# Performance work log

Measured on AMD Instinct MI355X. Metric: run time of the kernel, lower is better.

## Reference

```python
import jax, jax.numpy as jnp
from jax import lax
import numpy as np

H = 256  # hidden_size


def gru_last(x, Wih, Whh, bih, bhh):
    """Single-layer torch-convention GRU; returns last hidden state.
    x: [B, T, C] -> [B, H]"""
    B, T, _ = x.shape
    h_dim = Whh.shape[1]
    xW = x @ Wih.T + bih  # [B, T, 3H], precompute input gates
    def step(h, xw):
        gi_r, gi_z, gi_n = jnp.split(xw, 3, axis=-1)
        gh = h @ Whh.T + bhh
        gh_r, gh_z, gh_n = jnp.split(gh, 3, axis=-1)
        r = jax.nn.sigmoid(gi_r + gh_r)
        z = jax.nn.sigmoid(gi_z + gh_z)
        n = jnp.tanh(gi_n + r * gh_n)
        return (1.0 - z) * n + z * h, None
    h0 = jnp.zeros((B, h_dim), x.dtype)
    hT, _ = lax.scan(step, h0, jnp.swapaxes(xW, 0, 1))
    return hT


def setup_inputs() -> dict:
    key = jax.random.key(0)
    ks = jax.random.split(key, 16)
    B, N, M, C, C1 = 32, 64, 64, 64, 16
    inter = 2 * H + 6 * C + C1  # 912
    s = 0.05
    x1 = jax.random.normal(ks[0], (B, N, C1), jnp.float32)
    states = jax.random.normal(ks[1], (B, N, M, C), jnp.float32)
    perm1 = jax.vmap(lambda k: jax.random.permutation(k, M))(jax.random.split(ks[2], N)).astype(jnp.int64)
    perm2 = jax.vmap(lambda k: jax.random.permutation(k, N))(jax.random.split(ks[3], N)).astype(jnp.int64)
    return {
        "x1": x1, "states": states, "perm1": perm1, "perm2": perm2,
        # shared 2D->1D GRU (ModuleList([gru]*2) shares parameters)
        "gru2d_Wih": jax.random.normal(ks[4], (3 * H, C), jnp.float32) * s,
        "gru2d_Whh": jax.random.normal(ks[5], (3 * H, H), jnp.float32) * s,
        "gru2d_bih": jax.random.normal(ks[6], (3 * H,), jnp.float32) * s,
        "gru2d_bhh": jax.random.normal(ks[7], (3 * H,), jnp.float32) * s,
        "gru1d_Wih": jax.random.normal(ks[8], (3 * H, inter), jnp.float32) * s,
        "gru1d_Whh": jax.random.normal(ks[9], (3 * H, H), jnp.float32) * s,
        "gru1d_bih": jax.random.normal(ks[10], (3 * H,), jnp.float32) * s,
        "gru1d_bhh": jax.random.normal(ks[11], (3 * H,), jnp.float32) * s,
        "fc1_W": jax.random.normal(ks[12], (H, 3 * inter + H), jnp.float32) * s,
        "fc1_b": jax.random.normal(ks[13], (H,), jnp.float32) * s,
        "fc2_W": jax.random.normal(ks[14], (1, H), jnp.float32) * s,
        "fc2_b": jax.random.normal(ks[15], (1,), jnp.float32) * s,
    }


def reference(x1, states, perm1, perm2,
              gru2d_Wih, gru2d_Whh, gru2d_bih, gru2d_bhh,
              gru1d_Wih, gru1d_Whh, gru1d_bih, gru1d_bhh,
              fc1_W, fc1_b, fc2_W, fc2_b):
    B, N, M, C = states.shape
    d = [states.max(1), states.mean(1), states.min(1),   # [B, M, C] each (N==M)
         states.max(2), states.mean(2), states.min(2)]   # [B, N, C] each
    idx = jnp.arange(N)[:, None]
    # g1[b,i,t,c] = states[b, i, perm1[i,t], c]
    g1 = states[:, idx, perm1, :]                         # [B, N, M, C]
    # g2[b,i,t,c] = states[b, perm2[i,t], i, c]
    g2 = states[:, perm2, idx, :]                         # [B, N, N, C]
    sd1 = gru_last(g1.reshape(B * N, M, C), gru2d_Wih, gru2d_Whh, gru2d_bih, gru2d_bhh).reshape(B, N, H)
    sd2 = gru_last(g2.reshape(B * N, N, C), gru2d_Wih, gru2d_Whh, gru2d_bih, gru2d_bhh).reshape(B, N, H)
    f = jnp.concatenate(d + [sd1, sd2], axis=2)           # [B, N, 6C + 2H]
    f = jnp.concatenate([x1, f], axis=-1)                 # [B, N, inter]
    hlast = gru_last(f, gru1d_Wih, gru1d_Whh, gru1d_bih, gru1d_bhh)  # [B, H]
    g = jnp.concatenate([f.max(1), f.mean(1), f.min(1), hlast], axis=1)
    h = jax.nn.relu(g @ fc1_W.T + fc1_b)
    out = h @ fc2_W.T + fc2_b
    return out.reshape(B)
```

## Files before the change

### kernel.cpp

```cpp
#include <hip/hip_runtime.h>
#include <cmath>

#define B_ 32
#define N_ 64
#define H_ 256
#define G3_ 768
#define INTER_ 912
#define KP_ 928
#define FCIN_ 2992
#define GRED_ 2736

#define PADA 264
#define PADX 72

typedef __attribute__((ext_vector_type(8))) short short8;
typedef __attribute__((ext_vector_type(4))) short sshort4;
typedef __attribute__((ext_vector_type(4))) float float4v;

#define MFMA __builtin_amdgcn_mfma_f32_16x16x32_bf16

__device__ __forceinline__ float sigmoid_f(float x) {
    return __builtin_amdgcn_rcpf(1.0f + __builtin_amdgcn_exp2f(-1.44269504f * x));
}
__device__ __forceinline__ float tanh_fast(float x) {
    return 1.0f - 2.0f * __builtin_amdgcn_rcpf(1.0f + __builtin_amdgcn_exp2f(2.88539008f * x));
}
__device__ __forceinline__ unsigned f2bf_bits(float x) {
    unsigned u = __float_as_uint(x);
    return (u + 0x7fffu + ((u >> 16) & 1u)) >> 16;
}
__device__ __forceinline__ short f2bf(float x) { return (short)f2bf_bits(x); }

__global__ __launch_bounds__(256) void prep_kernel(
        const float* __restrict__ Whh2, const float* __restrict__ Wih2,
        const float* __restrict__ Whh1, const float* __restrict__ Wih1,
        const float* __restrict__ fc1W,
        short* __restrict__ Bfrag, short* __restrict__ Bfrag1,
        short* __restrict__ Bfrag1W, float* __restrict__ fc1Wt) {
    int idx = blockIdx.x * 256 + threadIdx.x;
    if (idx < 10 * 48 * 64 * 8) {
        int j = idx & 7, lane = (idx >> 3) & 63, tile = idx >> 9;
        int nt = tile % 48, kt = tile / 48;
        int n = nt * 16 + (lane & 15);
        int kb = (lane >> 4) * 8 + j;
        float v = (kt < 8) ? Whh2[n * 256 + kt * 32 + kb]
                           : Wih2[n * 64 + (kt - 8) * 32 + kb];
        Bfrag[idx] = f2bf(v);
    }
    if (idx < 8 * 48 * 64 * 8) {
        int j = idx & 7, lane = (idx >> 3) & 63, tile = idx >> 9;
        int nt = tile % 48, kt = tile / 48;
        int n = nt * 16 + (lane & 15);
        int k = kt * 32 + (lane >> 4) * 8 + j;
        Bfrag1[idx] = f2bf(Whh1[n * 256 + k]);
    }
    if (idx < 29 * 48 * 64 * 8) {
        int j = idx & 7, lane = (idx >> 3) & 63, tile = idx >> 9;
        int nt = tile % 48, kt = tile / 48;
        int n = nt * 16 + (lane & 15);
        int k = kt * 32 + (lane >> 4) * 8 + j;
        Bfrag1W[idx] = (k < INTER_) ? f2bf(Wih1[n * INTER_ + k]) : (short)0;
    }
    if (idx < FCIN_ * 256) {
        int o = idx & 255, i = idx >> 8;
        fc1Wt[idx] = fc1W[o * FCIN_ + i];
    }
}

__global__ __launch_bounds__(256) void reduce_states_kernel(
        const float* __restrict__ states, const float* __restrict__ x1,
        float* __restrict__ f) {
    const int c = threadIdx.x & 63;
    const int bj = blockIdx.x * 4 + (threadIdx.x >> 6);
    const int b = bj >> 6, j = bj & 63;
    const float* p1 = states + b * 262144 + j * 64 + c;
    const float* p2 = states + b * 262144 + j * 4096 + c;
    float mx1 = -1e30f, mn1 = 1e30f, sm1 = 0.f;
    float mx2 = -1e30f, mn2 = 1e30f, sm2 = 0.f;
    #pragma unroll 8
    for (int n = 0; n < 64; ++n) {
        float v = __builtin_nontemporal_load(p1 + n * 4096);
        mx1 = fmaxf(mx1, v); mn1 = fminf(mn1, v); sm1 += v;
    }
    #pragma unroll 8
    for (int m = 0; m < 64; ++m) {
        float v = __builtin_nontemporal_load(p2 + m * 64);
        mx2 = fmaxf(mx2, v); mn2 = fminf(mn2, v); sm2 += v;
    }
    float* fr = f + bj * INTER_;
    fr[16 + c]  = mx1;  fr[80 + c]  = sm1 * (1.f / 64.f);  fr[144 + c] = mn1;
    fr[208 + c] = mx2;  fr[272 + c] = sm2 * (1.f / 64.f);  fr[336 + c] = mn2;
    if (c < 16) fr[c] = x1[bj * 16 + c];
}

__global__ __launch_bounds__(512, 1) void gru2d_mfma(
        const float* __restrict__ states,
        const int* __restrict__ perm1, const int* __restrict__ perm2,
        const short* __restrict__ Bfrag,
        const float* __restrict__ bih, const float* __restrict__ bhh,
        float* __restrict__ f) {
    __shared__ short hA[2][16 * PADA];
    __shared__ short xA[2][16 * PADX];
    __shared__ short8 Blds[2 * 48 * 64];
    __shared__ int perms[1024];

    const int tid = threadIdx.x;
    const int lane = tid & 63;
    const int w = tid >> 6;
    const int m = lane & 15;
    const int q = lane >> 4;
    const bool sd2 = blockIdx.x >= 128;
    const int sblock = (blockIdx.x & 127) * 16;

    for (int i = tid; i < 1024; i += 512) {
        int r = i >> 6, t = i & 63;
        int qq = (sblock + r) & 63;
        perms[i] = sd2 ? perm2[qq * 64 + t] : perm1[qq * 64 + t];
    }
    for (int i = tid; i < 16 * PADA; i += 512) hA[0][i] = 0;
    {
        const uint4* src = (const uint4*)(Bfrag + 6 * 48 * 64 * 8);
        uint4* dst = (uint4*)Blds;
        #pragma unroll
        for (int rep = 0; rep < 12; ++rep)
            dst[tid + rep * 512] = src[tid + rep * 512];
    }

    const short8* Bf8 = (const short8*)Bfrag;
    short8 Bres[36];
    #pragma unroll
    for (int kt = 0; kt < 6; ++kt)
        #pragma unroll
        for (int j = 0; j < 6; ++j)
            Bres[kt * 6 + j] = Bf8[(kt * 48 + 8 * j + w) * 64 + lane];

    short8 Bx[12];
    #pragma unroll
    for (int kt = 0; kt < 2; ++kt)
        #pragma unroll
        for (int j = 0; j < 6; ++j)
            Bx[kt * 6 + j] = Bf8[((8 + kt) * 48 + 8 * j + w) * 64 + lane];

    const int u0 = 16 * w + m;
    const int u1 = 128 + u0;
    const float br0 = bih[u0] + bhh[u0],             br1 = bih[u1] + bhh[u1];
    const float bz0 = bih[256 + u0] + bhh[256 + u0], bz1 = bih[256 + u1] + bhh[256 + u1];
    const float bnx0 = bih[512 + u0], bnx1 = bih[512 + u1];
    const float bnh0 = bhh[512 + u0], bnh1 = bhh[512 + u1];

    float4v hreg0 = {0.f, 0.f, 0.f, 0.f}, hreg1 = {0.f, 0.f, 0.f, 0.f};

    {
        #pragma unroll
        for (int half = 0; half < 2; ++half) {
            int i = tid + half * 512;
            int r = i >> 6, c = i & 63;
            int s = sblock + r, b = s >> 6, qq = s & 63;
            int p = perms[r * 64 + 0];
            int src = sd2 ? ((b * 64 + p) * 64 + qq) * 64 + c
                          : ((b * 64 + qq) * 64 + p) * 64 + c;
            xA[0][r * PADX + c] = f2bf(states[src]);
        }
    }
    __syncthreads();

    for (int t = 0; t < 64; ++t) {
        const short* hAc = hA[t & 1];
        const short* xAc = xA[t & 1];

        float xg0 = 0.f, xg1 = 0.f;
        int w0 = -1, w1 = -1;
        if (t + 1 < 64) {
            #pragma unroll
            for (int half = 0; half < 2; ++half) {
                int i = tid + half * 512;
                int r = i >> 6, c = i & 63;
                int s = sblock + r, b = s >> 6, qq = s & 63;
                int p = perms[r * 64 + t + 1];
                int src = sd2 ? ((b * 64 + p) * 64 + qq) * 64 + c
                              : ((b * 64 + qq) * 64 + p) * 64 + c;
                float v = states[src];
                if (half == 0) { xg0 = v; w0 = r * PADX + c; }
                else           { xg1 = v; w1 = r * PADX + c; }
            }
        }

        float4v aR0 = {br0, br0, br0, br0},     aR1 = {br1, br1, br1, br1};
        float4v aZ0 = {bz0, bz0, bz0, bz0},     aZ1 = {bz1, bz1, bz1, bz1};
        float4v aNh0 = {bnh0, bnh0, bnh0, bnh0}, aNh1 = {bnh1, bnh1, bnh1, bnh1};
        float4v aNx0 = {bnx0, bnx0, bnx0, bnx0}, aNx1 = {bnx1, bnx1, bnx1, bnx1};

        #pragma unroll
        for (int kt = 0; kt < 6; ++kt) {
            short8 a = *(const short8*)(hAc + m * PADA + kt * 32 + q * 8);
            aR0  = MFMA(a, Bres[kt * 6 + 0], aR0, 0, 0, 0);
            aR1  = MFMA(a, Bres[kt * 6 + 1], aR1, 0, 0, 0);
            aZ0  = MFMA(a, Bres[kt * 6 + 2], aZ0, 0, 0, 0);
            aZ1  = MFMA(a, Bres[kt * 6 + 3], aZ1, 0, 0, 0);
            aNh0 = MFMA(a, Bres[kt * 6 + 4], aNh0, 0, 0, 0);
            aNh1 = MFMA(a, Bres[kt * 6 + 5], aNh1, 0, 0, 0);
        }
        #pragma unroll
        for (int kt = 0; kt < 2; ++kt) {
            short8 a = *(const short8*)(hAc + m * PADA + (6 + kt) * 32 + q * 8);
            short8 b0 = Blds[(kt * 48 + 8 * 0 + w) * 64 + lane];
            short8 b1 = Blds[(kt * 48 + 8 * 1 + w) * 64 + lane];
            short8 b2 = Blds[(kt * 48 + 8 * 2 + w) * 64 + lane];
            short8 b3 = Blds[(kt * 48 + 8 * 3 + w) * 64 + lane];
            short8 b4 = Blds[(kt * 48 + 8 * 4 + w) * 64 + lane];
            short8 b5 = Blds[(kt * 48 + 8 * 5 + w) * 64 + lane];
            aR0  = MFMA(a, b0, aR0, 0, 0, 0);
            aR1  = MFMA(a, b1, aR1, 0, 0, 0);
            aZ0  = MFMA(a, b2, aZ0, 0, 0, 0);
            aZ1  = MFMA(a, b3, aZ1, 0, 0, 0);
            aNh0 = MFMA(a, b4, aNh0, 0, 0, 0);
            aNh1 = MFMA(a, b5, aNh1, 0, 0, 0);
        }
        #pragma unroll
        for (int kt = 0; kt < 2; ++kt) {
            short8 a = *(const short8*)(xAc + m * PADX + kt * 32 + q * 8);
            aR0  = MFMA(a, Bx[kt * 6 + 0], aR0, 0, 0, 0);
            aR1  = MFMA(a, Bx[kt * 6 + 1], aR1, 0, 0, 0);
            aZ0  = MFMA(a, Bx[kt * 6 + 2], aZ0, 0, 0, 0);
            aZ1  = MFMA(a, Bx[kt * 6 + 3], aZ1, 0, 0, 0);
            aNx0 = MFMA(a, Bx[kt * 6 + 4], aNx0, 0, 0, 0);
            aNx1 = MFMA(a, Bx[kt * 6 + 5], aNx1, 0, 0, 0);
        }

        short* hAn = hA[(t + 1) & 1];
        #pragma unroll
        for (int p = 0; p < 4; ++p) {
            int row = q * 4 + p;
            float r0 = sigmoid_f(aR0[p]);
            float z0 = sigmoid_f(aZ0[p]);
            float n0 = tanh_fast(aNx0[p] + r0 * aNh0[p]);
            float h0 = n0 + z0 * (hreg0[p] - n0);
            hreg0[p] = h0;
            hAn[row * PADA + u0] = f2bf(h0);
            float r1 = sigmoid_f(aR1[p]);
            float z1 = sigmoid_f(aZ1[p]);
            float n1 = tanh_fast(aNx1[p] + r1 * aNh1[p]);
            float h1 = n1 + z1 * (hreg1[p] - n1);
            hreg1[p] = h1;
            hAn[row * PADA + u1] = f2bf(h1);
        }
        if (t + 1 < 64) {
            xA[(t + 1) & 1][w0] = f2bf(xg0);
            xA[(t + 1) & 1][w1] = f2bf(xg1);
        }
        __syncthreads();
    }

    const int off = sd2 ? 656 : 400;
    #pragma unroll
    for (int p = 0; p < 4; ++p) {
        int s = sblock + q * 4 + p;
        f[s * INTER_ + off + u0] = hreg0[p];
        f[s * INTER_ + off + u1] = hreg1[p];
    }
}

__global__ __launch_bounds__(256) void convert_f_kernel(
        const float* __restrict__ f, short* __restrict__ fbf) {
    int idx = blockIdx.x * 256 + threadIdx.x;
    int row = idx / 232;
    int c4 = (idx - row * 232) * 4;
    if (row >= 2048) return;
    sshort4 o;
    if (c4 < INTER_) {
        float4v v = *(const float4v*)(f + row * INTER_ + c4);
        o[0] = f2bf(v[0]); o[1] = f2bf(v[1]); o[2] = f2bf(v[2]); o[3] = f2bf(v[3]);
    } else {
        o[0] = 0; o[1] = 0; o[2] = 0; o[3] = 0;
    }
    *(sshort4*)(fbf + row * KP_ + c4) = o;
}

__global__ __launch_bounds__(256) void gemm_xw1_mfma(
        const short* __restrict__ fbf, const short* __restrict__ BfragW,
        const float* __restrict__ bih, float* __restrict__ xw) {
    const int tid = threadIdx.x;
    const int lane = tid & 63;
    const int w = tid >> 6;
    const int m = lane & 15;
    const int q = lane >> 4;
    const int tn = blockIdx.x;
    const int tm = blockIdx.y;
    const int rowb = tm * 64 + w * 16;
    const short8* Bf8 = (const short8*)BfragW;

    float4v acc[4];
    #pragma unroll
    for (int nn = 0; nn < 4; ++nn) {
        float b = bih[tn * 64 + nn * 16 + m];
        acc[nn][0] = b; acc[nn][1] = b; acc[nn][2] = b; acc[nn][3] = b;
    }

    const short* arow = fbf + (rowb + m) * KP_;
    short8 a_cur = *(const short8*)(arow + q * 8);
    short8 b_cur[4];
    #pragma unroll
    for (int nn = 0; nn < 4; ++nn)
        b_cur[nn] = Bf8[(tn * 4 + nn) * 64 + lane];

    for (int kt = 0; kt < 29; ++kt) {
        short8 a_nxt = a_cur;
        short8 b_nxt[4];
        if (kt + 1 < 29) {
            a_nxt = *(const short8*)(arow + (kt + 1) * 32 + q * 8);
            #pragma unroll
            for (int nn = 0; nn < 4; ++nn)
                b_nxt[nn] = Bf8[((kt + 1) * 48 + tn * 4 + nn) * 64 + lane];
        }
        #pragma unroll
        for (int nn = 0; nn < 4; ++nn)
            acc[nn] = MFMA(a_cur, b_cur[nn], acc[nn], 0, 0, 0);
        a_cur = a_nxt;
        #pragma unroll
        for (int nn = 0; nn < 4; ++nn) b_cur[nn] = b_nxt[nn];
    }

    #pragma unroll
    for (int p = 0; p < 4; ++p) {
        int row = rowb + q * 4 + p;
        int seq = row >> 6, t = row & 63;
        #pragma unroll
        for (int nn = 0; nn < 4; ++nn)
            xw[(t * 32 + seq) * G3_ + tn * 64 + nn * 16 + m] = acc[nn][p];
    }
}

__global__ __launch_bounds__(512, 1) void gru1d_freduce(
        const float* __restrict__ xw, const short* __restrict__ Bfrag1,
        const float* __restrict__ bhh, float* __restrict__ hlast,
        const float* __restrict__ f, float* __restrict__ g) {
    __shared__ short hA[2][16 * PADA];
    __shared__ short8 Blds[2 * 48 * 64];

    const int tid = threadIdx.x;

    if (blockIdx.x >= 2) {
        const int b = blockIdx.x - 2;
        for (int i = tid; i < INTER_; i += 512) {
            const float* fp = f + (size_t)(b * 64) * INTER_ + i;
            float mx = -1e30f, mn = 1e30f, sm = 0.f;
            #pragma unroll 8
            for (int t = 0; t < 64; ++t) {
                float v = __builtin_nontemporal_load(fp + t * INTER_);
                mx = fmaxf(mx, v); mn = fminf(mn, v); sm += v;
            }
            g[b * GRED_ + i] = mx;
            g[b * GRED_ + INTER_ + i] = sm * (1.f / 64.f);
            g[b * GRED_ + 2 * INTER_ + i] = mn;
        }
        return;
    }

    const int lane = tid & 63;
    const int w = tid >> 6;
    const int m = lane & 15;
    const int q = lane >> 4;
    const int sblock = blockIdx.x * 16;

    for (int i = tid; i < 16 * PADA; i += 512) hA[0][i] = 0;
    {
        const uint4* src = (const uint4*)(Bfrag1 + 6 * 48 * 64 * 8);
        uint4* dst = (uint4*)Blds;
        #pragma unroll
        for (int rep = 0; rep < 12; ++rep)
            dst[tid + rep * 512] = src[tid + rep * 512];
    }
    const short8* Bf8 = (const short8*)Bfrag1;
    short8 Bres[36];
    #pragma unroll
    for (int kt = 0; kt < 6; ++kt)
        #pragma unroll
        for (int j = 0; j < 6; ++j)
            Bres[kt * 6 + j] = Bf8[(kt * 48 + 8 * j + w) * 64 + lane];

    const int u0 = 16 * w + m;
    const int u1 = 128 + u0;
    const float br0 = bhh[u0],       br1 = bhh[u1];
    const float bz0 = bhh[256 + u0], bz1 = bhh[256 + u1];
    const float bn0 = bhh[512 + u0], bn1 = bhh[512 + u1];

    float4v hreg0 = {0.f, 0.f, 0.f, 0.f}, hreg1 = {0.f, 0.f, 0.f, 0.f};
    __syncthreads();

    for (int t = 0; t < 64; ++t) {
        const short* hAc = hA[t & 1];

        float giR0[4], giR1[4], giZ0[4], giZ1[4], giN0[4], giN1[4];
        #pragma unroll
        for (int p = 0; p < 4; ++p) {
            const float* gr = xw + (size_t)(t * 32 + sblock + q * 4 + p) * G3_;
            giR0[p] = gr[u0];        giR1[p] = gr[u1];
            giZ0[p] = gr[256 + u0];  giZ1[p] = gr[256 + u1];
            giN0[p] = gr[512 + u0];  giN1[p] = gr[512 + u1];
        }

        float4v aR0 = {br0, br0, br0, br0}, aR1 = {br1, br1, br1, br1};
        float4v aZ0 = {bz0, bz0, bz0, bz0}, aZ1 = {bz1, bz1, bz1, bz1};
        float4v aN0 = {bn0, bn0, bn0, bn0}, aN1 = {bn1, bn1, bn1, bn1};

        #pragma unroll
        for (int kt = 0; kt < 6; ++kt) {
            short8 a = *(const short8*)(hAc + m * PADA + kt * 32 + q * 8);
            aR0 = MFMA(a, Bres[kt * 6 + 0], aR0, 0, 0, 0);
            aR1 = MFMA(a, Bres[kt * 6 + 1], aR1, 0, 0, 0);
            aZ0 = MFMA(a, Bres[kt * 6 + 2], aZ0, 0, 0, 0);
            aZ1 = MFMA(a, Bres[kt * 6 + 3], aZ1, 0, 0, 0);
            aN0 = MFMA(a, Bres[kt * 6 + 4], aN0, 0, 0, 0);
            aN1 = MFMA(a, Bres[kt * 6 + 5], aN1, 0, 0, 0);
        }
        #pragma unroll
        for (int kt = 0; kt < 2; ++kt) {
            short8 a = *(const short8*)(hAc + m * PADA + (6 + kt) * 32 + q * 8);
            short8 b0 = Blds[(kt * 48 + 8 * 0 + w) * 64 + lane];
            short8 b1 = Blds[(kt * 48 + 8 * 1 + w) * 64 + lane];
            short8 b2 = Blds[(kt * 48 + 8 * 2 + w) * 64 + lane];
            short8 b3 = Blds[(kt * 48 + 8 * 3 + w) * 64 + lane];
            short8 b4 = Blds[(kt * 48 + 8 * 4 + w) * 64 + lane];
            short8 b5 = Blds[(kt * 48 + 8 * 5 + w) * 64 + lane];
            aR0 = MFMA(a, b0, aR0, 0, 0, 0);
            aR1 = MFMA(a, b1, aR1, 0, 0, 0);
            aZ0 = MFMA(a, b2, aZ0, 0, 0, 0);
            aZ1 = MFMA(a, b3, aZ1, 0, 0, 0);
            aN0 = MFMA(a, b4, aN0, 0, 0, 0);
            aN1 = MFMA(a, b5, aN1, 0, 0, 0);
        }

        short* hAn = hA[(t + 1) & 1];
        #pragma unroll
        for (int p = 0; p < 4; ++p) {
            int row = q * 4 + p;
            float r0 = sigmoid_f(giR0[p] + aR0[p]);
            float z0 = sigmoid_f(giZ0[p] + aZ0[p]);
            float n0 = tanh_fast(giN0[p] + r0 * aN0[p]);
            float h0 = n0 + z0 * (hreg0[p] - n0);
            hreg0[p] = h0;
            hAn[row * PADA + u0] = f2bf(h0);
            float r1 = sigmoid_f(giR1[p] + aR1[p]);
            float z1 = sigmoid_f(giZ1[p] + aZ1[p]);
            float n1 = tanh_fast(giN1[p] + r1 * aN1[p]);
            float h1 = n1 + z1 * (hreg1[p] - n1);
            hreg1[p] = h1;
            hAn[row * PADA + u1] = f2bf(h1);
        }
        __syncthreads();
    }

    #pragma unroll
    for (int p = 0; p < 4; ++p) {
        int s = sblock + q * 4 + p;
        hlast[s * 256 + u0] = hreg0[p];
        hlast[s * 256 + u1] = hreg1[p];
    }
}

__global__ __launch_bounds__(256) void tail_fc(
        const float* __restrict__ g, const float* __restrict__ hlast,
        const float* __restrict__ fc1Wt, const float* __restrict__ fc1b,
        const float* __restrict__ fc2W, const float* __restrict__ fc2b,
        float* __restrict__ out) {
    __shared__ float g_lds[FCIN_];
    __shared__ float red[4];
    const int tid = threadIdx.x;
    const int b = blockIdx.x;
    for (int i = tid; i < GRED_; i += 256) g_lds[i] = g[b * GRED_ + i];
    g_lds[GRED_ + tid] = hlast[b * 256 + tid];
    __syncthreads();

    float a0 = 0.f, a1 = 0.f, a2 = 0.f, a3 = 0.f;
    for (int i = 0; i < FCIN_; i += 4) {
        a0 = fmaf(g_lds[i],     fc1Wt[(i) * 256 + tid],     a0);
        a1 = fmaf(g_lds[i + 1], fc1Wt[(i + 1) * 256 + tid], a1);
        a2 = fmaf(g_lds[i + 2], fc1Wt[(i + 2) * 256 + tid], a2);
        a3 = fmaf(g_lds[i + 3], fc1Wt[(i + 3) * 256 + tid], a3);
    }
    float acc = ((a0 + a1) + (a2 + a3)) + fc1b[tid];
    float hv = fmaxf(acc, 0.f);
    float part = hv * fc2W[tid];
    #pragma unroll
    for (int off = 32; off >= 1; off >>= 1)
        part += __shfl_down(part, off, 64);
    if ((tid & 63) == 0) red[tid >> 6] = part;
    __syncthreads();
    if (tid == 0)
        out[b] = fc2b[0] + red[0] + red[1] + red[2] + red[3];
}

extern "C" void kernel_launch(void* const* d_in, const int* in_sizes, int n_in,
                              void* d_out, int out_size, void* d_ws, size_t ws_size,
                              hipStream_t stream) {
    const float* x1     = (const float*)d_in[0];
    const float* states = (const float*)d_in[1];
    const int*   perm1  = (const int*)d_in[2];
    const int*   perm2  = (const int*)d_in[3];
    const float* Wih2   = (const float*)d_in[4];
    const float* Whh2   = (const float*)d_in[5];
    const float* bih2   = (const float*)d_in[6];
    const float* bhh2   = (const float*)d_in[7];
    const float* Wih1   = (const float*)d_in[8];
    const float* Whh1   = (const float*)d_in[9];
    const float* bih1   = (const float*)d_in[10];
    const float* bhh1   = (const float*)d_in[11];
    const float* fc1W   = (const float*)d_in[12];
    const float* fc1b   = (const float*)d_in[13];
    const float* fc2W   = (const float*)d_in[14];
    const float* fc2b   = (const float*)d_in[15];
    float* out = (float*)d_out;

    float* ws = (float*)d_ws;
    short* Bfrag   = (short*)ws;
    short* Bfrag1  = (short*)(ws + 122880);
    short* Bfrag1W = (short*)(ws + 122880 + 98304);
    float* fc1Wt   = ws + 577536;
    float* f       = fc1Wt + FCIN_ * 256;
    short* fbf     = (short*)(f + 2048 * INTER_);
    float* xw1     = f + 2048 * INTER_ + 950272;
    float* hlast   = xw1 + 2048 * G3_;
    float* g       = hlast + 8192;

    prep_kernel<<<dim3(2992), 256, 0, stream>>>(Whh2, Wih2, Whh1, Wih1, fc1W,
                                                Bfrag, Bfrag1, Bfrag1W, fc1Wt);
    reduce_states_kernel<<<dim3(512), 256, 0, stream>>>(states, x1, f);
    gru2d_mfma<<<dim3(256), 512, 0, stream>>>(states, perm1, perm2, Bfrag,
                                              bih2, bhh2, f);
    convert_f_kernel<<<dim3(1856), 256, 0, stream>>>(f, fbf);
    gemm_xw1_mfma<<<dim3(12, 32), 256, 0, stream>>>(fbf, Bfrag1W, bih1, xw1);
    gru1d_freduce<<<dim3(34), 512, 0, stream>>>(xw1, Bfrag1, bhh1, hlast, f, g);
    tail_fc<<<dim3(32), 256, 0, stream>>>(g, hlast, fc1Wt, fc1b, fc2W, fc2b, out);
}
```

Baseline: 637.1 us.

## Interleave sd1 and sd2 GRU recurrences in one block to overlap epilogues with MFMA

Each block now runs two independent 2D GRU sequences (the perm1 and perm2 directions) in alternating half-steps. The gate epilogue of one sequence is spread between the MFMA k-tiles of the other, so transcendental math hides behind matrix work. The x input is packed into the same LDS A-buffer as the hidden state, and some weight fragments are streamed from global memory per k-tile instead of being held in registers. The grid shrinks from 256 to 128 blocks, so fewer CUs are used and each block does twice the sequential work, betting that overlap outweighs the lost parallelism.

```diff
diff --git a/kernel.cpp b/kernel.cpp
--- a/kernel.cpp
+++ b/kernel.cpp
@@ -11,7 +11,7 @@
 #define GRED_ 2736
 
 #define PADA 264
-#define PADX 72
+#define PADA2 328
 
 typedef __attribute__((ext_vector_type(8))) short short8;
 typedef __attribute__((ext_vector_type(4))) short sshort4;
@@ -93,33 +93,49 @@
     if (c < 16) fr[c] = x1[bj * 16 + c];
 }
 
+#define EPI_STEP(P, aR0v, aR1v, aZ0v, aZ1v, aNh0v, aNh1v, aNx0v, aNx1v, hr0, hr1, dst) \
+    do {                                                                     \
+        const int row_ = q * 4 + (P);                                        \
+        float r0_ = sigmoid_f(aR0v[P]);                                      \
+        float z0_ = sigmoid_f(aZ0v[P]);                                      \
+        float n0_ = tanh_fast(aNx0v[P] + r0_ * aNh0v[P]);                    \
+        float h0_ = n0_ + z0_ * (hr0[P] - n0_);                              \
+        hr0[P] = h0_;                                                        \
+        (dst)[row_ * PADA2 + u0] = f2bf(h0_);                                \
+        float r1_ = sigmoid_f(aR1v[P]);                                      \
+        float z1_ = sigmoid_f(aZ1v[P]);                                      \
+        float n1_ = tanh_fast(aNx1v[P] + r1_ * aNh1v[P]);                    \
+        float h1_ = n1_ + z1_ * (hr1[P] - n1_);                              \
+        hr1[P] = h1_;                                                        \
+        (dst)[row_ * PADA2 + u1] = f2bf(h1_);                                \
+    } while (0)
+
 __global__ __launch_bounds__(512, 1) void gru2d_mfma(
         const float* __restrict__ states,
         const int* __restrict__ perm1, const int* __restrict__ perm2,
         const short* __restrict__ Bfrag,
         const float* __restrict__ bih, const float* __restrict__ bhh,
         float* __restrict__ f) {
-    __shared__ short hA[2][16 * PADA];
-    __shared__ short xA[2][16 * PADX];
+    __shared__ short hA[2][16 * PADA2];
     __shared__ short8 Blds[2 * 48 * 64];
-    __shared__ int perms[1024];
+    __shared__ int perms[2][1024];
 
     const int tid = threadIdx.x;
     const int lane = tid & 63;
     const int w = tid >> 6;
     const int m = lane & 15;
     const int q = lane >> 4;
-    const bool sd2 = blockIdx.x >= 128;
-    const int sblock = (blockIdx.x & 127) * 16;
-
-    for (int i = tid; i < 1024; i += 512) {
-        int r = i >> 6, t = i & 63;
+    const int sblock = blockIdx.x * 16;
+
+    for (int i = tid; i < 2048; i += 512) {
+        int grp = i >> 10, idx = i & 1023;
+        int r = idx >> 6, t = idx & 63;
         int qq = (sblock + r) & 63;
-        perms[i] = sd2 ? perm2[qq * 64 + t] : perm1[qq * 64 + t];
-    }
-    for (int i = tid; i < 16 * PADA; i += 512) hA[0][i] = 0;
+        perms[grp][idx] = grp ? perm2[qq * 64 + t] : perm1[qq * 64 + t];
+    }
+    for (int i = tid; i < 2 * 16 * PADA2; i += 512) ((short*)hA)[i] = 0;
     {
-        const uint4* src = (const uint4*)(Bfrag + 6 * 48 * 64 * 8);
+        const uint4* src = (const uint4*)(Bfrag + 4 * 48 * 64 * 8);
         uint4* dst = (uint4*)Blds;
         #pragma unroll
         for (int rep = 0; rep < 12; ++rep)
@@ -127,19 +143,12 @@
     }
 
     const short8* Bf8 = (const short8*)Bfrag;
-    short8 Bres[36];
-    #pragma unroll
-    for (int kt = 0; kt < 6; ++kt)
+    short8 Bres[24];
+    #pragma unroll
+    for (int kt = 0; kt < 4; ++kt)
         #pragma unroll
         for (int j = 0; j < 6; ++j)
             Bres[kt * 6 + j] = Bf8[(kt * 48 + 8 * j + w) * 64 + lane];
-
-    short8 Bx[12];
-    #pragma unroll
-    for (int kt = 0; kt < 2; ++kt)
-        #pragma unroll
-        for (int j = 0; j < 6; ++j)
-            Bx[kt * 6 + j] = Bf8[((8 + kt) * 48 + 8 * j + w) * 64 + lane];
 
     const int u0 = 16 * w + m;
     const int u1 = 128 + u0;
@@ -148,115 +157,227 @@
     const float bnx0 = bih[512 + u0], bnx1 = bih[512 + u1];
     const float bnh0 = bhh[512 + u0], bnh1 = bhh[512 + u1];
 
-    float4v hreg0 = {0.f, 0.f, 0.f, 0.f}, hreg1 = {0.f, 0.f, 0.f, 0.f};
+    const int s0g = sblock + w,     b0g = s0g >> 6, qq0 = s0g & 63;
+    const int s1g = sblock + w + 8, b1g = s1g >> 6, qq1 = s1g & 63;
+    const float* baseA0 = states + (size_t)(b0g * 64 + qq0) * 4096 + lane;
+    const float* baseA1 = states + (size_t)(b1g * 64 + qq1) * 4096 + lane;
+    const float* baseB0 = states + (size_t)b0g * 262144 + qq0 * 64 + lane;
+    const float* baseB1 = states + (size_t)b1g * 262144 + qq1 * 64 + lane;
+    const int w0o = w * PADA2 + 256 + lane;
+    const int w1o = (w + 8) * PADA2 + 256 + lane;
+
+    float4v hrA0 = {0,0,0,0}, hrA1 = {0,0,0,0};
+    float4v hrB0 = {0,0,0,0}, hrB1 = {0,0,0,0};
+    float4v AR0, AR1, AZ0, AZ1, ANh0, ANh1, ANx0, ANx1;
+    float4v BR0, BR1, BZ0, BZ1, BNh0, BNh1, BNx0, BNx1;
+    float xgA0, xgA1, xgB0 = 0.f, xgB1 = 0.f;
+
+    __syncthreads();
+    hA[0][w0o] = f2bf(baseA0[perms[0][w * 64] * 64]);
+    hA[0][w1o] = f2bf(baseA1[perms[0][(w + 8) * 64] * 64]);
+    hA[1][w0o] = f2bf(baseB0[perms[1][w * 64] * 4096]);
+    hA[1][w1o] = f2bf(baseB1[perms[1][(w + 8) * 64] * 4096]);
+    __syncthreads();
+
+    #pragma unroll 1
+    for (int e = 0; e < 64; ++e) {
+        {
+            const short* hAc = (const short*)hA[0];
+            short* hBd = (short*)hA[1];
+            AR0  = (float4v){br0, br0, br0, br0};
+            AR1  = (float4v){br1, br1, br1, br1};
+            AZ0  = (float4v){bz0, bz0, bz0, bz0};
+            AZ1  = (float4v){bz1, bz1, bz1, bz1};
+            ANh0 = (float4v){bnh0, bnh0, bnh0, bnh0};
+            ANh1 = (float4v){bnh1, bnh1, bnh1, bnh1};
+            ANx0 = (float4v){bnx0, bnx0, bnx0, bnx0};
+            ANx1 = (float4v){bnx1, bnx1, bnx1, bnx1};
+            if (e < 63) {
+                xgA0 = baseA0[perms[0][w * 64 + e + 1] * 64];
+                xgA1 = baseA1[perms[0][(w + 8) * 64 + e + 1] * 64];
+            }
+            short8 bR6[6], bR7[6], bR8[6], bR9[6];
+            #pragma unroll
+            for (int kt = 0; kt < 10; ++kt) {
+                short8 a = *(const short8*)(hAc + m * PADA2 + kt * 32 + q * 8);
+                short8 b0, b1, b2, b3, b4, b5;
+                if (kt < 4) {
+                    b0 = Bres[kt * 6 + 0]; b1 = Bres[kt * 6 + 1];
+                    b2 = Bres[kt * 6 + 2]; b3 = Bres[kt * 6 + 3];
+                    b4 = Bres[kt * 6 + 4]; b5 = Bres[kt * 6 + 5];
+                } else if (kt < 6) {
+                    b0 = Blds[((kt - 4) * 48 + 8 * 0 + w) * 64 + lane];
+                    b1 = Blds[((kt - 4) * 48 + 8 * 1 + w) * 64 + lane];
+                    b2 = Blds[((kt - 4) * 48 + 8 * 2 + w) * 64 + lane];
+                    b3 = Blds[((kt - 4) * 48 + 8 * 3 + w) * 64 + lane];
+                    b4 = Blds[((kt - 4) * 48 + 8 * 4 + w) * 64 + lane];
+                    b5 = Blds[((kt - 4) * 48 + 8 * 5 + w) * 64 + lane];
+                } else if (kt == 6) {
+                    b0 = bR6[0]; b1 = bR6[1]; b2 = bR6[2];
+                    b3 = bR6[3]; b4 = bR6[4]; b5 = bR6[5];
+                } else if (kt == 7) {
+                    b0 = bR7[0]; b1 = bR7[1]; b2 = bR7[2];
+                    b3 = bR7[3]; b4 = bR7[4]; b5 = bR7[5];
+                } else if (kt == 8) {
+                    b0 = bR8[0]; b1 = bR8[1]; b2 = bR8[2];
+                    b3 = bR8[3]; b4 = bR8[4]; b5 = bR8[5];
+                } else {
+                    b0 = bR9[0]; b1 = bR9[1]; b2 = bR9[2];
+                    b3 = bR9[3]; b4 = bR9[4]; b5 = bR9[5];
+                }
+                AR0 = MFMA(a, b0, AR0, 0, 0, 0);
+                AR1 = MFMA(a, b1, AR1, 0, 0, 0);
+                AZ0 = MFMA(a, b2, AZ0, 0, 0, 0);
+                AZ1 = MFMA(a, b3, AZ1, 0, 0, 0);
+                if (kt < 8) {
+                    ANh0 = MFMA(a, b4, ANh0, 0, 0, 0);
+                    ANh1 = MFMA(a, b5, ANh1, 0, 0, 0);
+                } else {
+                    ANx0 = MFMA(a, b4, ANx0, 0, 0, 0);
+                    ANx1 = MFMA(a, b5, ANx1, 0, 0, 0);
+                }
+                if (kt == 3) {
+                    #pragma unroll
+                    for (int j = 0; j < 6; ++j)
+                        bR6[j] = Bf8[(6 * 48 + 8 * j + w) * 64 + lane];
+                }
+                if (kt == 4) {
+                    #pragma unroll
+                    for (int j = 0; j < 6; ++j)
+                        bR7[j] = Bf8[(7 * 48 + 8 * j + w) * 64 + lane];
+                }
+                if (kt == 5) {
+                    #pragma unroll
+                    for (int j = 0; j < 6; ++j)
+                        bR8[j] = Bf8[(8 * 48 + 8 * j + w) * 64 + lane];
+                }
+                if (kt == 6) {
+                    #pragma unroll
+                    for (int j = 0; j < 6; ++j)
+                        bR9[j] = Bf8[(9 * 48 + 8 * j + w) * 64 + lane];
+                }
+                if (kt == 1 && e > 0)
+                    EPI_STEP(0, BR0, BR1, BZ0, BZ1, BNh0, BNh1, BNx0, BNx1, hrB0, hrB1, hBd);
+                if (kt == 3 && e > 0)
+                    EPI_STEP(1, BR0, BR1, BZ0, BZ1, BNh0, BNh1, BNx0, BNx1, hrB0, hrB1, hBd);
+                if (kt == 5 && e > 0)
+                    EPI_STEP(2, BR0, BR1, BZ0, BZ1, BNh0, BNh1, BNx0, BNx1, hrB0, hrB1, hBd);
+                if (kt == 7 && e > 0)
+                    EPI_STEP(3, BR0, BR1, BZ0, BZ1, BNh0, BNh1, BNx0, BNx1, hrB0, hrB1, hBd);
+            }
+            if (e > 0) {
+                hBd[w0o] = f2bf(xgB0);
+                hBd[w1o] = f2bf(xgB1);
+            }
+        }
+        __syncthreads();
+        {
+            const short* hBc = (const short*)hA[1];
+            short* hAd = (short*)hA[0];
+            BR0  = (float4v){br0, br0, br0, br0};
+            BR1  = (float4v){br1, br1, br1, br1};
+            BZ0  = (float4v){bz0, bz0, bz0, bz0};
+            BZ1  = (float4v){bz1, bz1, bz1, bz1};
+            BNh0 = (float4v){bnh0, bnh0, bnh0, bnh0};
+            BNh1 = (float4v){bnh1, bnh1, bnh1, bnh1};
+            BNx0 = (float4v){bnx0, bnx0, bnx0, bnx0};
+            BNx1 = (float4v){bnx1, bnx1, bnx1, bnx1};
+            if (e < 63) {
+                xgB0 = baseB0[perms[1][w * 64 + e + 1] * 4096];
+                xgB1 = baseB1[perms[1][(w + 8) * 64 + e + 1] * 4096];
+            }
+            short8 bR6[6], bR7[6], bR8[6], bR9[6];
+            #pragma unroll
+            for (int kt = 0; kt < 10; ++kt) {
+                short8 a = *(const short8*)(hBc + m * PADA2 + kt * 32 + q * 8);
+                short8 b0, b1, b2, b3, b4, b5;
+                if (kt < 4) {
+                    b0 = Bres[kt * 6 + 0]; b1 = Bres[kt * 6 + 1];
+                    b2 = Bres[kt * 6 + 2]; b3 = Bres[kt * 6 + 3];
+                    b4 = Bres[kt * 6 + 4]; b5 = Bres[kt * 6 + 5];
+                } else if (kt < 6) {
+                    b0 = Blds[((kt - 4) * 48 + 8 * 0 + w) * 64 + lane];
+                    b1 = Blds[((kt - 4) * 48 + 8 * 1 + w) * 64 + lane];
+                    b2 = Blds[((kt - 4) * 48 + 8 * 2 + w) * 64 + lane];
+                    b3 = Blds[((kt - 4) * 48 + 8 * 3 + w) * 64 + lane];
+                    b4 = Blds[((kt - 4) * 48 + 8 * 4 + w) * 64 + lane];
+                    b5 = Blds[((kt - 4) * 48 + 8 * 5 + w) * 64 + lane];
+                } else if (kt == 6) {
+                    b0 = bR6[0]; b1 = bR6[1]; b2 = bR6[2];
+                    b3 = bR6[3]; b4 = bR6[4]; b5 = bR6[5];
+                } else if (kt == 7) {
+                    b0 = bR7[0]; b1 = bR7[1]; b2 = bR7[2];
+                    b3 = bR7[3]; b4 = bR7[4]; b5 = bR7[5];
+                } else if (kt == 8) {
+                    b0 = bR8[0]; b1 = bR8[1]; b2 = bR8[2];
+                    b3 = bR8[3]; b4 = bR8[4]; b5 = bR8[5];
+                } else {
+                    b0 = bR9[0]; b1 = bR9[1]; b2 = bR9[2];
+                    b3 = bR9[3]; b4 = bR9[4]; b5 = bR9[5];
+                }
+                BR0 = MFMA(a, b0, BR0, 0, 0, 0);
+                BR1 = MFMA(a, b1, BR1, 0, 0, 0);
+                BZ0 = MFMA(a, b2, BZ0, 0, 0, 0);
+                BZ1 = MFMA(a, b3, BZ1, 0, 0, 0);
+                if (kt < 8) {
+                    BNh0 = MFMA(a, b4, BNh0, 0, 0, 0);
+                    BNh1 = MFMA(a, b5, BNh1, 0, 0, 0);
+                } else {
+                    BNx0 = MFMA(a, b4, BNx0, 0, 0, 0);
+                    BNx1 = MFMA(a, b5, BNx1, 0, 0, 0);
+                }
+                if (kt == 3) {
+                    #pragma unroll
+                    for (int j = 0; j < 6; ++j)
+                        bR6[j] = Bf8[(6 * 48 + 8 * j + w) * 64 + lane];
+                }
+                if (kt == 4) {
+                    #pragma unroll
+                    for (int j = 0; j < 6; ++j)
+                        bR7[j] = Bf8[(7 * 48 + 8 * j + w) * 64 + lane];
+                }
+                if (kt == 5) {
+                    #pragma unroll
+                    for (int j = 0; j < 6; ++j)
+                        bR8[j] = Bf8[(8 * 48 + 8 * j + w) * 64 + lane];
+                }
+                if (kt == 6) {
+                    #pragma unroll
+                    for (int j = 0; j < 6; ++j)
+                        bR9[j] = Bf8[(9 * 48 + 8 * j + w) * 64 + lane];
+                }
+                if (kt == 1)
+                    EPI_STEP(0, AR0, AR1, AZ0, AZ1, ANh0, ANh1, ANx0, ANx1, hrA0, hrA1, hAd);
+                if (kt == 3)
+                    EPI_STEP(1, AR0, AR1, AZ0, AZ1, ANh0, ANh1, ANx0, ANx1, hrA0, hrA1, hAd);
+                if (kt == 5)
+                    EPI_STEP(2, AR0, AR1, AZ0, AZ1, ANh0, ANh1, ANx0, ANx1, hrA0, hrA1, hAd);
+                if (kt == 7)
+                    EPI_STEP(3, AR0, AR1, AZ0, AZ1, ANh0, ANh1, ANx0, ANx1, hrA0, hrA1, hAd);
+            }
+            if (e < 63) {
+                hAd[w0o] = f2bf(xgA0);
+                hAd[w1o] = f2bf(xgA1);
+            }
+        }
+        __syncthreads();
+    }
 
     {
-        #pragma unroll
-        for (int half = 0; half < 2; ++half) {
-            int i = tid + half * 512;
-            int r = i >> 6, c = i & 63;
-            int s = sblock + r, b = s >> 6, qq = s & 63;
-            int p = perms[r * 64 + 0];
-            int src = sd2 ? ((b * 64 + p) * 64 + qq) * 64 + c
-                          : ((b * 64 + qq) * 64 + p) * 64 + c;
-            xA[0][r * PADX + c] = f2bf(states[src]);
-        }
-    }
-    __syncthreads();
-
-    for (int t = 0; t < 64; ++t) {
-        const short* hAc = hA[t & 1];
-        const short* xAc = xA[t & 1];
-
-        float xg0 = 0.f, xg1 = 0.f;
-        int w0 = -1, w1 = -1;
-        if (t + 1 < 64) {
-            #pragma unroll
-            for (int half = 0; half < 2; ++half) {
-                int i = tid + half * 512;
-                int r = i >> 6, c = i & 63;
-                int s = sblock + r, b = s >> 6, qq = s & 63;
-                int p = perms[r * 64 + t + 1];
-                int src = sd2 ? ((b * 64 + p) * 64 + qq) * 64 + c
-                              : ((b * 64 + qq) * 64 + p) * 64 + c;
-                float v = states[src];
-                if (half == 0) { xg0 = v; w0 = r * PADX + c; }
-                else           { xg1 = v; w1 = r * PADX + c; }
-            }
-        }
-
-        float4v aR0 = {br0, br0, br0, br0},     aR1 = {br1, br1, br1, br1};
-        float4v aZ0 = {bz0, bz0, bz0, bz0},     aZ1 = {bz1, bz1, bz1, bz1};
-        float4v aNh0 = {bnh0, bnh0, bnh0, bnh0}, aNh1 = {bnh1, bnh1, bnh1, bnh1};
-        float4v aNx0 = {bnx0, bnx0, bnx0, bnx0}, aNx1 = {bnx1, bnx1, bnx1, bnx1};
-
-        #pragma unroll
-        for (int kt = 0; kt < 6; ++kt) {
-            short8 a = *(const short8*)(hAc + m * PADA + kt * 32 + q * 8);
-            aR0  = MFMA(a, Bres[kt * 6 + 0], aR0, 0, 0, 0);
-            aR1  = MFMA(a, Bres[kt * 6 + 1], aR1, 0, 0, 0);
-            aZ0  = MFMA(a, Bres[kt * 6 + 2], aZ0, 0, 0, 0);
-            aZ1  = MFMA(a, Bres[kt * 6 + 3], aZ1, 0, 0, 0);
-            aNh0 = MFMA(a, Bres[kt * 6 + 4], aNh0, 0, 0, 0);
-            aNh1 = MFMA(a, Bres[kt * 6 + 5], aNh1, 0, 0, 0);
-        }
-        #pragma unroll
-        for (int kt = 0; kt < 2; ++kt) {
-            short8 a = *(const short8*)(hAc + m * PADA + (6 + kt) * 32 + q * 8);
-            short8 b0 = Blds[(kt * 48 + 8 * 0 + w) * 64 + lane];
-            short8 b1 = Blds[(kt * 48 + 8 * 1 + w) * 64 + lane];
-            short8 b2 = Blds[(kt * 48 + 8 * 2 + w) * 64 + lane];
-            short8 b3 = Blds[(kt * 48 + 8 * 3 + w) * 64 + lane];
-            short8 b4 = Blds[(kt * 48 + 8 * 4 + w) * 64 + lane];
-            short8 b5 = Blds[(kt * 48 + 8 * 5 + w) * 64 + lane];
-            aR0  = MFMA(a, b0, aR0, 0, 0, 0);
-            aR1  = MFMA(a, b1, aR1, 0, 0, 0);
-            aZ0  = MFMA(a, b2, aZ0, 0, 0, 0);
-            aZ1  = MFMA(a, b3, aZ1, 0, 0, 0);
-            aNh0 = MFMA(a, b4, aNh0, 0, 0, 0);
-            aNh1 = MFMA(a, b5, aNh1, 0, 0, 0);
-        }
-        #pragma unroll
-        for (int kt = 0; kt < 2; ++kt) {
-            short8 a = *(const short8*)(xAc + m * PADX + kt * 32 + q * 8);
-            aR0  = MFMA(a, Bx[kt * 6 + 0], aR0, 0, 0, 0);
-            aR1  = MFMA(a, Bx[kt * 6 + 1], aR1, 0, 0, 0);
-            aZ0  = MFMA(a, Bx[kt * 6 + 2], aZ0, 0, 0, 0);
-            aZ1  = MFMA(a, Bx[kt * 6 + 3], aZ1, 0, 0, 0);
-            aNx0 = MFMA(a, Bx[kt * 6 + 4], aNx0, 0, 0, 0);
-            aNx1 = MFMA(a, Bx[kt * 6 + 5], aNx1, 0, 0, 0);
-        }
-
-        short* hAn = hA[(t + 1) & 1];
-        #pragma unroll
-        for (int p = 0; p < 4; ++p) {
-            int row = q * 4 + p;
-            float r0 = sigmoid_f(aR0[p]);
-            float z0 = sigmoid_f(aZ0[p]);
-            float n0 = tanh_fast(aNx0[p] + r0 * aNh0[p]);
-            float h0 = n0 + z0 * (hreg0[p] - n0);
-            hreg0[p] = h0;
-            hAn[row * PADA + u0] = f2bf(h0);
-            float r1 = sigmoid_f(aR1[p]);
-            float z1 = sigmoid_f(aZ1[p]);
-            float n1 = tanh_fast(aNx1[p] + r1 * aNh1[p]);
-            float h1 = n1 + z1 * (hreg1[p] - n1);
-            hreg1[p] = h1;
-            hAn[row * PADA + u1] = f2bf(h1);
-        }
-        if (t + 1 < 64) {
-            xA[(t + 1) & 1][w0] = f2bf(xg0);
-            xA[(t + 1) & 1][w1] = f2bf(xg1);
-        }
-        __syncthreads();
-    }
-
-    const int off = sd2 ? 656 : 400;
+        short* hBd = (short*)hA[1];
+        EPI_STEP(0, BR0, BR1, BZ0, BZ1, BNh0, BNh1, BNx0, BNx1, hrB0, hrB1, hBd);
+        EPI_STEP(1, BR0, BR1, BZ0, BZ1, BNh0, BNh1, BNx0, BNx1, hrB0, hrB1, hBd);
+        EPI_STEP(2, BR0, BR1, BZ0, BZ1, BNh0, BNh1, BNx0, BNx1, hrB0, hrB1, hBd);
+        EPI_STEP(3, BR0, BR1, BZ0, BZ1, BNh0, BNh1, BNx0, BNx1, hrB0, hrB1, hBd);
+    }
+
     #pragma unroll
     for (int p = 0; p < 4; ++p) {
         int s = sblock + q * 4 + p;
-        f[s * INTER_ + off + u0] = hreg0[p];
-        f[s * INTER_ + off + u1] = hreg1[p];
+        f[s * INTER_ + 400 + u0] = hrA0[p];
+        f[s * INTER_ + 400 + u1] = hrA1[p];
+        f[s * INTER_ + 656 + u0] = hrB0[p];
+        f[s * INTER_ + 656 + u1] = hrB1[p];
     }
 }
 
@@ -525,7 +646,7 @@
     prep_kernel<<<dim3(2992), 256, 0, stream>>>(Whh2, Wih2, Whh1, Wih1, fc1W,
                                                 Bfrag, Bfrag1, Bfrag1W, fc1Wt);
     reduce_states_kernel<<<dim3(512), 256, 0, stream>>>(states, x1, f);
-    gru2d_mfma<<<dim3(256), 512, 0, stream>>>(states, perm1, perm2, Bfrag,
+    gru2d_mfma<<<dim3(128), 512, 0, stream>>>(states, perm1, perm2, Bfrag,
                                               bih2, bhh2, f);
     convert_f_kernel<<<dim3(1856), 256, 0, stream>>>(f, fbf);
     gemm_xw1_mfma<<<dim3(12, 32), 256, 0, stream>>>(fbf, Bfrag1W, bih1, xw1);
```

Result: slower. 1.110 ms (+74.2%).
